# Kernel tuning notes

Measured on AMD Instinct MI355X. Metric: run time of the kernel, lower is better.

Reference implementation:

```python
import jax, jax.numpy as jnp
import numpy as np

THRESH = 0.5   # spike threshold
LENS = 0.5     # surrogate-gradient window half-width
DECAY = 0.2    # membrane leak factor

@jax.custom_vjp
def act_fun(u):
    # Heaviside spike with rectangular surrogate gradient (matches torch ActFun)
    return (u > THRESH).astype(u.dtype)

def _act_fwd(u):
    return act_fun(u), u

def _act_bwd(u, g):
    return (g * (jnp.abs(u - THRESH) < LENS).astype(g.dtype),)

act_fun.defvjp(_act_fwd, _act_bwd)


def setup_inputs() -> dict:
    key = jax.random.key(0)
    # [batch, features, time]
    x = jax.random.normal(key, (128, 4096, 100), dtype=jnp.float32)
    return {"x": x}


def reference(x):
    # x: [..., T]; LIF scan over the last (time) axis.
    xt = jnp.moveaxis(x, -1, 0)  # [T, ...]
    init_mem = jnp.zeros(x.shape[:-1], dtype=x.dtype)
    init_spike = jnp.zeros(x.shape[:-1], dtype=x.dtype)  # out[...,0] is zero before step 0 write

    def step(carry, xi):
        mem, spike = carry
        mem = mem * DECAY * (1.0 - spike) + xi
        spike = act_fun(mem)
        return (mem, spike), spike

    _, out = jax.lax.scan(step, (init_mem, init_spike), xt)  # out: [T, ...]
    return jnp.moveaxis(out, 0, -1)
```

## Files before the change

kernel.cpp:

```cpp
#include <hip/hip_runtime.h>


#define THRESH 0.5f
#define DECAY  0.2f

constexpr int T        = 100;
constexpr int ROWS     = 64;
constexpr int F4_ROW   = T / 4;
constexpr int F4_TILE  = ROWS * F4_ROW;
constexpr int K        = F4_TILE / 64;
constexpr int STRIDE   = ROWS + 1;

__global__ __launch_bounds__(64) void lif_kernel(const float* __restrict__ x,
                                                 float* __restrict__ out) {
    __shared__ float4 tile[F4_ROW * STRIDE];

    const int l = threadIdx.x;
    const size_t base = (size_t)blockIdx.x * F4_TILE;
    const float4* src = reinterpret_cast<const float4*>(x) + base;
    float4*       dst = reinterpret_cast<float4*>(out) + base;

    float4 v[K];
#pragma unroll
    for (int k = 0; k < K; ++k) v[k] = src[k * 64 + l];
#pragma unroll
    for (int k = 0; k < K; ++k) {
        int flat = k * 64 + l;
        int r = flat / F4_ROW;
        int g = flat % F4_ROW;
        tile[g * STRIDE + r] = v[k];
    }
    __syncthreads();

    float mem = 0.0f, spike = 0.0f;
#pragma unroll
    for (int g = 0; g < F4_ROW; ++g) {
        float4 u = tile[g * STRIDE + l];
        float4 s;
#define STEP(comp)                                                            \
        {                                                                     \
            float leak = __fmul_rn(mem, DECAY);                               \
            mem = (spike != 0.0f) ? u.comp : __fadd_rn(leak, u.comp);         \
            spike = (mem > THRESH) ? 1.0f : 0.0f;                             \
            s.comp = spike;                                                   \
        }
        STEP(x) STEP(y) STEP(z) STEP(w)
#undef STEP
        tile[g * STRIDE + l] = s;
    }
    __syncthreads();

#pragma unroll
    for (int k = 0; k < K; ++k) {
        int flat = k * 64 + l;
        int r = flat / F4_ROW;
        int g = flat % F4_ROW;
        dst[k * 64 + l] = tile[g * STRIDE + r];
    }
}

extern "C" void kernel_launch(void* const* d_in, const int* in_sizes, int n_in,
                              void* d_out, int out_size, void* d_ws, size_t ws_size,
                              hipStream_t stream) {
    const float* x   = (const float*)d_in[0];
    float*       out = (float*)d_out;

    int n_neurons = in_sizes[0] / T;
    int grid = n_neurons / ROWS;

    lif_kernel<<<grid, ROWS, 0, stream>>>(x, out);
}
```

Measured before the change: 344.3 us.

## Persistent grid with register prefetch of next tile overlapping compute

Replaces the one-tile-per-block launch with a fixed persistent grid in which each block loops over tiles. Each block prefetches the next tile's global loads into registers while it runs the scan and stores for the current tile, and relies on wavefront-level LDS waitcnt instead of __syncthreads since blocks are a single wave. This is meant to hide global load latency and cut block launch overhead. In exchange it reduces the number of resident waves, which lowers latency hiding from occupancy, and it is correct only because each block is exactly one wave.

```diff
diff --git a/kernel.cpp b/kernel.cpp
--- a/kernel.cpp
+++ b/kernel.cpp
@@ -10,52 +10,82 @@
 constexpr int F4_TILE  = ROWS * F4_ROW;
 constexpr int K        = F4_TILE / 64;
 constexpr int STRIDE   = ROWS + 1;
+constexpr int GRID     = 1536;
+
+#define WAIT_LGKM0() __builtin_amdgcn_s_waitcnt(0xC07F)
 
 __global__ __launch_bounds__(64) void lif_kernel(const float* __restrict__ x,
-                                                 float* __restrict__ out) {
+                                                 float* __restrict__ out,
+                                                 int ntiles) {
     __shared__ float4 tile[F4_ROW * STRIDE];
 
     const int l = threadIdx.x;
-    const size_t base = (size_t)blockIdx.x * F4_TILE;
-    const float4* src = reinterpret_cast<const float4*>(x) + base;
-    float4*       dst = reinterpret_cast<float4*>(out) + base;
+    const float4* xf = reinterpret_cast<const float4*>(x);
+    float4*       of = reinterpret_cast<float4*>(out);
+
+    int t = blockIdx.x;
+    if (t >= ntiles) return;
 
     float4 v[K];
+
+    {
+        const float4* src = xf + (size_t)t * F4_TILE;
 #pragma unroll
-    for (int k = 0; k < K; ++k) v[k] = src[k * 64 + l];
+        for (int k = 0; k < K; ++k) v[k] = src[k * 64 + l];
 #pragma unroll
-    for (int k = 0; k < K; ++k) {
-        int flat = k * 64 + l;
-        int r = flat / F4_ROW;
-        int g = flat % F4_ROW;
-        tile[g * STRIDE + r] = v[k];
+        for (int k = 0; k < K; ++k) {
+            int f = k * 64 + l;
+            tile[(f % F4_ROW) * STRIDE + (f / F4_ROW)] = v[k];
+        }
     }
-    __syncthreads();
 
-    float mem = 0.0f, spike = 0.0f;
+    for (; t < ntiles; ) {
+        const int tn = t + GRID;
+        const bool have_next = (tn < ntiles);
+
+        if (have_next) {
+            const float4* src = xf + (size_t)tn * F4_TILE;
 #pragma unroll
-    for (int g = 0; g < F4_ROW; ++g) {
-        float4 u = tile[g * STRIDE + l];
-        float4 s;
+            for (int k = 0; k < K; ++k) v[k] = src[k * 64 + l];
+        }
+
+        WAIT_LGKM0();
+
+        float mem = 0.0f, spike = 0.0f;
+#pragma unroll
+        for (int g = 0; g < F4_ROW; ++g) {
+            float4 u = tile[g * STRIDE + l];
+            float4 s;
 #define STEP(comp)                                                            \
-        {                                                                     \
-            float leak = __fmul_rn(mem, DECAY);                               \
-            mem = (spike != 0.0f) ? u.comp : __fadd_rn(leak, u.comp);         \
-            spike = (mem > THRESH) ? 1.0f : 0.0f;                             \
-            s.comp = spike;                                                   \
+            {                                                                 \
+                float leak = __fmul_rn(mem, DECAY);                           \
+                mem = (spike != 0.0f) ? u.comp : __fadd_rn(leak, u.comp);     \
+                spike = (mem > THRESH) ? 1.0f : 0.0f;                         \
+                s.comp = spike;                                               \
+            }
+            STEP(x) STEP(y) STEP(z) STEP(w)
+#undef STEP
+            tile[g * STRIDE + l] = s;
         }
-        STEP(x) STEP(y) STEP(z) STEP(w)
-#undef STEP
-        tile[g * STRIDE + l] = s;
-    }
-    __syncthreads();
 
+        {
+            float4* dst = of + (size_t)t * F4_TILE;
 #pragma unroll
-    for (int k = 0; k < K; ++k) {
-        int flat = k * 64 + l;
-        int r = flat / F4_ROW;
-        int g = flat % F4_ROW;
-        dst[k * 64 + l] = tile[g * STRIDE + r];
+            for (int k = 0; k < K; ++k) {
+                int f = k * 64 + l;
+                dst[k * 64 + l] = tile[(f % F4_ROW) * STRIDE + (f / F4_ROW)];
+            }
+        }
+
+        if (have_next) {
+#pragma unroll
+            for (int k = 0; k < K; ++k) {
+                int f = k * 64 + l;
+                tile[(f % F4_ROW) * STRIDE + (f / F4_ROW)] = v[k];
+            }
+        }
+
+        t = tn;
     }
 }
 
@@ -66,7 +96,7 @@
     float*       out = (float*)d_out;
 
     int n_neurons = in_sizes[0] / T;
-    int grid = n_neurons / ROWS;
+    int ntiles    = n_neurons / ROWS;
 
-    lif_kernel<<<grid, ROWS, 0, stream>>>(x, out);
+    lif_kernel<<<GRID, ROWS, 0, stream>>>(x, out, ntiles);
 }
```

After: 381.6 us. +10.8%, slower.
